# Optimization experiments

Measured on AMD Instinct MI355X. Metric: run time of the kernel, lower is better.

Reference implementation:

```python
import jax, jax.numpy as jnp
import numpy as np

N_BOXES = 1_000_000
EPS = 1e-6


def box2corners(box):
    """(..., 5) [x,y,w,h,angle] -> (..., 4, 2) corners (mmcv box2corners)."""
    x, y, w, h, a = (box[..., i] for i in range(5))
    dx = jnp.asarray([0.5, -0.5, -0.5, 0.5], box.dtype) * w[..., None]  # (...,4)
    dy = jnp.asarray([0.5, 0.5, -0.5, -0.5], box.dtype) * h[..., None]
    cos, sin = jnp.cos(a)[..., None], jnp.sin(a)[..., None]
    cx = dx * cos - dy * sin + x[..., None]
    cy = dx * sin + dy * cos + y[..., None]
    return jnp.stack([cx, cy], axis=-1)


def box_intersection(c1, c2):
    """All 4x4 edge-pair segment intersections. c1,c2: (N,4,2).
    Returns pts (N,4,4,2), mask (N,4,4)."""
    roll = jnp.array([1, 2, 3, 0])
    line1 = jnp.concatenate([c1, c1[:, roll, :]], axis=-1)  # (N,4,4): x1,y1,x2,y2
    line2 = jnp.concatenate([c2, c2[:, roll, :]], axis=-1)
    l1 = line1[:, :, None, :]  # (N,4,1,4)
    l2 = line2[:, None, :, :]  # (N,1,4,4)
    x1, y1, x2, y2 = l1[..., 0], l1[..., 1], l1[..., 2], l1[..., 3]
    x3, y3, x4, y4 = l2[..., 0], l2[..., 1], l2[..., 2], l2[..., 3]
    num = (y4 - y3) * (x2 - x1) - (x4 - x3) * (y2 - y1)
    den_t = (x4 - x3) * (y1 - y3) - (y4 - y3) * (x1 - x3)
    safe = jnp.where(num == 0.0, 1.0, num)
    t = jnp.where(num == 0.0, -1.0, den_t / safe)
    mask_t = (t > 0) & (t < 1)
    den_u = (x2 - x1) * (y1 - y3) - (y2 - y1) * (x1 - x3)
    u = jnp.where(num == 0.0, -1.0, -den_u / safe)
    mask_u = (u > 0) & (u < 1)
    mask = mask_t & mask_u
    t2 = den_t / (num + 1e-8)
    pts = jnp.stack([x1 + t2 * (x2 - x1), y1 + t2 * (y2 - y1)], axis=-1)
    pts = pts * mask[..., None].astype(pts.dtype)
    return pts, mask


def box1_in_box2(c1, c2):
    """Which corners of c1 lie inside box c2. (N,4,2)x(N,4,2)->(N,4) bool."""
    a = c2[:, 0:1, :]
    b = c2[:, 1:2, :]
    d = c2[:, 3:4, :]
    ab, ad, am = b - a, d - a, c1 - a
    pab = jnp.sum(ab * am, -1) / jnp.sum(ab * ab, -1)
    pad_ = jnp.sum(ad * am, -1) / jnp.sum(ad * ad, -1)
    e = 1e-6
    return (pab > -e) & (pab < 1 + e) & (pad_ > -e) & (pad_ < 1 + e)


def intersection_area(c1, c2):
    """Differentiable rotated-box intersection area via convex polygon clipping."""
    inter_pts, inter_mask = box_intersection(c1, c2)
    m1 = box1_in_box2(c1, c2)
    m2 = box1_in_box2(c2, c1)
    n = c1.shape[0]
    verts = jnp.concatenate([c1, c2, inter_pts.reshape(n, 16, 2)], axis=1)  # (N,24,2)
    mask = jnp.concatenate([m1, m2, inter_mask.reshape(n, 16)], axis=1)     # (N,24)
    k = jnp.sum(mask, axis=-1)  # num valid vertices per box
    mf = mask.astype(verts.dtype)
    mean = jnp.sum(verts * mf[..., None], axis=1, keepdims=True) / \
        jnp.maximum(k, 1).astype(verts.dtype)[:, None, None]
    vn = verts - mean
    # sort valid vertices counterclockwise by angle around centroid; invalid last
    ang = jnp.where(mask, jnp.arctan2(vn[..., 1], vn[..., 0]), 1e9)
    order = jnp.argsort(ang, axis=-1)
    vs = jnp.take_along_axis(verts, order[..., None], axis=1)  # (N,24,2)
    idx = jnp.arange(24)
    nxt = jnp.where(idx[None, :] + 1 < k[:, None], idx[None, :] + 1, 0)
    v_next = jnp.take_along_axis(vs, nxt[..., None], axis=1)
    cross = vs[..., 0] * v_next[..., 1] - vs[..., 1] * v_next[..., 0]
    valid = idx[None, :] < k[:, None]
    return jnp.abs(jnp.sum(jnp.where(valid, cross, 0.0), axis=-1)) * 0.5


def fpdiou_loss(pred, target):
    c1 = box2corners(pred)
    c2 = box2corners(target)
    inter = intersection_area(c1, c2)
    area1 = pred[:, 2] * pred[:, 3]
    area2 = target[:, 2] * target[:, 3]
    iou = inter / (area1 + area2 - inter)
    iou = jnp.maximum(iou, EPS)
    # corner-distance term (detached in original via .detach().cpu().numpy())
    p = jax.lax.stop_gradient(c1)
    g = jax.lax.stop_gradient(c2)
    ps = jnp.take_along_axis(p, jnp.argsort(p[..., 0], axis=-1)[..., None], axis=1)
    gs = jnp.take_along_axis(g, jnp.argsort(g[..., 0], axis=-1)[..., None], axis=1)
    d = 2.0 * (gs[:, 0, 0] - ps[:, 0, 0]) ** 2 \
        + (ps[:, 1, 0] - gs[:, 1, 0]) ** 2 + (ps[:, 1, 1] - gs[:, 1, 1]) ** 2 \
        + (ps[:, 2, 0] - gs[:, 2, 0]) ** 2 + (ps[:, 2, 1] - gs[:, 2, 1]) ** 2 \
        + (ps[:, 3, 0] - gs[:, 3, 0]) ** 2 + (ps[:, 3, 1] - gs[:, 3, 1]) ** 2
    res = d / (4.0 * 1024.0 ** 2)
    loss = 1.0 - iou + res  # mode='linear'
    return jnp.mean(loss)   # reduction='mean', loss_weight=1.0


def setup_inputs() -> dict:
    key = jax.random.key(0)
    k1, k2, k3, k4 = jax.random.split(key, 4)
    xy = jax.random.uniform(k1, (N_BOXES, 2), minval=0.0, maxval=1024.0)
    wh = jax.random.uniform(k2, (N_BOXES, 2), minval=8.0, maxval=96.0)
    ang = jax.random.uniform(k3, (N_BOXES, 1), minval=-np.pi / 2, maxval=np.pi / 2)
    pred = jnp.concatenate([xy, wh, ang], axis=-1).astype(jnp.float32)
    scale = jnp.asarray([4.0, 4.0, 3.0, 3.0, 0.1], jnp.float32)
    target = pred + jax.random.normal(k4, (N_BOXES, 5), jnp.float32) * scale
    target = target.at[:, 2:4].set(jnp.maximum(target[:, 2:4], 4.0))
    return {"pred": pred, "target": target}


def reference(pred, target):
    return fpdiou_loss(pred, target)
```

## Files before the change

kernel.cpp:

```cpp
#include <hip/hip_runtime.h>

#define BS 256
#define NS 24

__device__ __forceinline__ float rcpf(float x) { return __builtin_amdgcn_rcpf(x); }

__device__ __forceinline__ unsigned pk16(float x, float y) {
    unsigned r;
    asm("v_cvt_pknorm_i16_f32 %0, %1, %2" : "=v"(r) : "v"(x), "v"(y));
    return r;
}

#define CSWAPK(A, B) do {                                         \
    const unsigned ka_ = key[A], kb_ = key[B];                    \
    key[A] = ka_ < kb_ ? ka_ : kb_;                               \
    key[B] = ka_ < kb_ ? kb_ : ka_;                               \
} while (0)

#define CSW2(x, y, I, J) do {                                     \
    const bool sw_ = (x[J] < x[I]);                               \
    const float xi_ = x[I], xj_ = x[J], yi_ = y[I], yj_ = y[J];   \
    x[I] = sw_ ? xj_ : xi_;  x[J] = sw_ ? xi_ : xj_;              \
    y[I] = sw_ ? yj_ : yi_;  y[J] = sw_ ? yi_ : yj_;              \
} while (0)

__global__ __launch_bounds__(BS, 4)
void fpdiou_kernel(const float* __restrict__ pred, const float* __restrict__ tgt,
                   float* __restrict__ out, int n, float inv_n)
{
    __shared__ unsigned s_p[NS * BS];
    __shared__ float s_red[BS / 64];

    const int tid = threadIdx.x;
    const int i = blockIdx.x * BS + tid;
    float loss = 0.f;

    if (i < n) {
        const float* pp = pred + (size_t)i * 5;
        const float* gg = tgt  + (size_t)i * 5;
        const float p0 = pp[0], p1 = pp[1], pw = pp[2], ph = pp[3], pa = pp[4];
        const float g0 = gg[0], g1 = gg[1], gw = gg[2], gh = gg[3], ga = gg[4];

        const float s1 = __sinf(pa), co1 = __cosf(pa);
        const float s2 = __sinf(ga), co2 = __cosf(ga);

        const float DX[4] = {0.5f, -0.5f, -0.5f, 0.5f};
        const float DY[4] = {0.5f,  0.5f, -0.5f, -0.5f};
        float c1x[4], c1y[4], c2x[4], c2y[4];
#pragma unroll
        for (int q = 0; q < 4; q++) {
            float dx = DX[q] * pw, dy = DY[q] * ph;
            c1x[q] = dx * co1 - dy * s1 + p0;
            c1y[q] = dx * s1 + dy * co1 + p1;
            dx = DX[q] * gw; dy = DY[q] * gh;
            c2x[q] = dx * co2 - dy * s2 + g0;
            c2y[q] = dx * s2 + dy * co2 + g1;
        }

        const float PKS = 128.f / 32767.f;

        float res;
        {
            float px_[4] = {c1x[0], c1x[1], c1x[2], c1x[3]};
            float py_[4] = {c1y[0], c1y[1], c1y[2], c1y[3]};
            float gx_[4] = {c2x[0], c2x[1], c2x[2], c2x[3]};
            float gy_[4] = {c2y[0], c2y[1], c2y[2], c2y[3]};
            CSW2(px_, py_, 0, 1); CSW2(px_, py_, 2, 3);
            CSW2(px_, py_, 0, 2); CSW2(px_, py_, 1, 3); CSW2(px_, py_, 1, 2);
            CSW2(gx_, gy_, 0, 1); CSW2(gx_, gy_, 2, 3);
            CSW2(gx_, gy_, 0, 2); CSW2(gx_, gy_, 1, 3); CSW2(gx_, gy_, 1, 2);
            const float d0 = gx_[0] - px_[0];
            float d = 2.f * d0 * d0;
#pragma unroll
            for (int q = 1; q < 4; q++) {
                const float dxq = px_[q] - gx_[q];
                const float dyq = py_[q] - gy_[q];
                d += dxq * dxq + dyq * dyq;
            }
            res = d * (1.f / 4194304.f);
        }

        unsigned vm = 0;
        float sx = 0.f, sy = 0.f;
        const float e = 1e-6f;

        {
            const float ax = c2x[0], ay = c2y[0];
            const float abx = c2x[1] - ax, aby = c2y[1] - ay;
            const float adx = c2x[3] - ax, ady = c2y[3] - ay;
            const float dab = abx * abx + aby * aby;
            const float dad = adx * adx + ady * ady;
            const float lo_ab = -e * dab, hi_ab = (1.f + e) * dab;
            const float lo_ad = -e * dad, hi_ad = (1.f + e) * dad;
#pragma unroll
            for (int q = 0; q < 4; q++) {
                const float amx = c1x[q] - ax, amy = c1y[q] - ay;
                const float dot_ab = abx * amx + aby * amy;
                const float dot_ad = adx * amx + ady * amy;
                const bool m = (dot_ab > lo_ab) & (dot_ab < hi_ab)
                             & (dot_ad > lo_ad) & (dot_ad < hi_ad);
                s_p[q * BS + tid] = pk16((c1x[q] - p0) * PKS, (c1y[q] - p1) * PKS);
                if (m) { vm |= 1u << q; sx += c1x[q]; sy += c1y[q]; }
            }
        }
        {
            const float ax = c1x[0], ay = c1y[0];
            const float abx = c1x[1] - ax, aby = c1y[1] - ay;
            const float adx = c1x[3] - ax, ady = c1y[3] - ay;
            const float dab = abx * abx + aby * aby;
            const float dad = adx * adx + ady * ady;
            const float lo_ab = -e * dab, hi_ab = (1.f + e) * dab;
            const float lo_ad = -e * dad, hi_ad = (1.f + e) * dad;
#pragma unroll
            for (int q = 0; q < 4; q++) {
                const float amx = c2x[q] - ax, amy = c2y[q] - ay;
                const float dot_ab = abx * amx + aby * amy;
                const float dot_ad = adx * amx + ady * amy;
                const bool m = (dot_ab > lo_ab) & (dot_ab < hi_ab)
                             & (dot_ad > lo_ad) & (dot_ad < hi_ad);
                s_p[(4 + q) * BS + tid] = pk16((c2x[q] - p0) * PKS, (c2y[q] - p1) * PKS);
                if (m) { vm |= 1u << (4 + q); sx += c2x[q]; sy += c2y[q]; }
            }
        }
        float iix[16], iiy[16];
#pragma unroll
        for (int a = 0; a < 4; a++) {
            const float x1 = c1x[a], y1 = c1y[a];
            const float ex = c1x[(a + 1) & 3] - x1, ey = c1y[(a + 1) & 3] - y1;
#pragma unroll
            for (int b = 0; b < 4; b++) {
                const float x3 = c2x[b], y3 = c2y[b];
                const float fx = c2x[(b + 1) & 3] - x3, fy = c2y[(b + 1) & 3] - y3;
                const float num = fy * ex - fx * ey;
                const float dx13 = x1 - x3, dy13 = y1 - y3;
                const float den_t = fx * dy13 - fy * dx13;
                const float den_u = ex * dy13 - ey * dx13;
                const bool m = (den_t * num > 0.f) & (fabsf(den_t) < fabsf(num))
                             & (den_u * num < 0.f) & (fabsf(den_u) < fabsf(num));
                const float t2 = den_t * rcpf(num + 1e-8f);
                const float ix = fmaf(t2, ex, x1), iy = fmaf(t2, ey, y1);
                const int s = 8 + a * 4 + b;
                iix[a * 4 + b] = ix; iiy[a * 4 + b] = iy;
                s_p[s * BS + tid] = pk16((ix - p0) * PKS, (iy - p1) * PKS);
                if (m) { vm |= 1u << s; sx += ix; sy += iy; }
            }
        }

        const int kq = __popc(vm);
        const float kf = (float)(kq > 0 ? kq : 1);
        const float mx = sx * rcpf(kf), my = sy * rcpf(kf);
        unsigned key[NS];
#pragma unroll
        for (int s = 0; s < NS; s++) {
            const float vx = (s < 4) ? c1x[s] : (s < 8) ? c2x[s - 4] : iix[s - 8];
            const float vy = (s < 4) ? c1y[s] : (s < 8) ? c2y[s - 4] : iiy[s - 8];
            const float dx = vx - mx, dy = vy - my;
            const float sa = fabsf(dx) + fabsf(dy);
            const float m1 = fmaf(-dx, rcpf(sa), 1.f);
            float a4 = copysignf(m1, dy) + 4.f;
            a4 = ((vm >> s) & 1u) ? a4 : 1e9f;
            key[s] = (__float_as_uint(a4) & 0xFFFFFFE0u) | (unsigned)s;
        }

        CSWAPK(0,16); CSWAPK(1,17); CSWAPK(2,18); CSWAPK(3,19);
        CSWAPK(4,20); CSWAPK(5,21); CSWAPK(6,22); CSWAPK(7,23);
        CSWAPK(0,8);  CSWAPK(1,9);  CSWAPK(2,10); CSWAPK(3,11);
        CSWAPK(4,12); CSWAPK(5,13); CSWAPK(6,14); CSWAPK(7,15);
        CSWAPK(8,16); CSWAPK(9,17); CSWAPK(10,18); CSWAPK(11,19);
        CSWAPK(12,20); CSWAPK(13,21); CSWAPK(14,22); CSWAPK(15,23);
        CSWAPK(0,4);  CSWAPK(1,5);  CSWAPK(2,6);  CSWAPK(3,7);
        CSWAPK(8,12); CSWAPK(9,13); CSWAPK(10,14); CSWAPK(11,15);
        CSWAPK(16,20); CSWAPK(17,21); CSWAPK(18,22); CSWAPK(19,23);
        CSWAPK(4,16); CSWAPK(5,17); CSWAPK(6,18); CSWAPK(7,19);
        CSWAPK(4,8);  CSWAPK(5,9);  CSWAPK(6,10); CSWAPK(7,11);
        CSWAPK(12,16); CSWAPK(13,17); CSWAPK(14,18); CSWAPK(15,19);
        CSWAPK(0,2);  CSWAPK(1,3);  CSWAPK(4,6);  CSWAPK(5,7);
        CSWAPK(8,10); CSWAPK(9,11); CSWAPK(12,14); CSWAPK(13,15);
        CSWAPK(16,18); CSWAPK(17,19); CSWAPK(20,22); CSWAPK(21,23);
        CSWAPK(2,16); CSWAPK(3,17); CSWAPK(6,20); CSWAPK(7,21);
        CSWAPK(2,8);  CSWAPK(3,9);  CSWAPK(6,12); CSWAPK(7,13);
        CSWAPK(10,16); CSWAPK(11,17); CSWAPK(14,20); CSWAPK(15,21);
        CSWAPK(2,4);  CSWAPK(3,5);  CSWAPK(6,8);  CSWAPK(7,9);
        CSWAPK(10,12); CSWAPK(11,13); CSWAPK(14,16); CSWAPK(15,17);
        CSWAPK(18,20); CSWAPK(19,21);
        CSWAPK(0,1);  CSWAPK(2,3);  CSWAPK(4,5);  CSWAPK(6,7);
        CSWAPK(8,9);  CSWAPK(10,11); CSWAPK(12,13); CSWAPK(14,15);
        CSWAPK(16,17); CSWAPK(18,19); CSWAPK(20,21); CSWAPK(22,23);
        CSWAPK(1,16); CSWAPK(3,18); CSWAPK(5,20); CSWAPK(7,22);
        CSWAPK(1,8);  CSWAPK(3,10); CSWAPK(5,12); CSWAPK(7,14);
        CSWAPK(9,16); CSWAPK(11,18); CSWAPK(13,20); CSWAPK(15,22);
        CSWAPK(1,4);  CSWAPK(3,6);  CSWAPK(5,8);  CSWAPK(7,10);
        CSWAPK(9,12); CSWAPK(11,14); CSWAPK(13,16); CSWAPK(15,18);
        CSWAPK(17,20); CSWAPK(19,22);
        CSWAPK(1,2);  CSWAPK(3,4);  CSWAPK(5,6);  CSWAPK(7,8);
        CSWAPK(9,10); CSWAPK(11,12); CSWAPK(13,14); CSWAPK(15,16);
        CSWAPK(17,18); CSWAPK(19,20); CSWAPK(21,22);

        const unsigned s0 = key[0] & 31u;
        unsigned wv[NS];
#pragma unroll
        for (int j = 0; j < NS; j++) {
            const unsigned slot = (key[j] < 0x4E000000u) ? (key[j] & 31u) : s0;
            wv[j] = s_p[slot * BS + tid];
        }
        float X[NS + 1], Y[NS + 1];
#pragma unroll
        for (int j = 0; j < NS; j++) {
            X[j] = (float)((int)(wv[j] << 16) >> 16);
            Y[j] = (float)((int)wv[j] >> 16);
        }
        X[NS] = X[0]; Y[NS] = Y[0];
        float cr0 = 0.f, cr1 = 0.f, cr2 = 0.f;
#pragma unroll
        for (int j = 0; j < NS; j++) {
            const float t = X[j] * Y[j + 1] - Y[j] * X[j + 1];
            if ((j % 3) == 0) cr0 += t; else if ((j % 3) == 1) cr1 += t; else cr2 += t;
        }
        const float cr = (cr0 + cr1) + cr2;
        const float area = fabsf(cr) * (0.5f / 16384.f);

        const float a1 = pw * ph, a2 = gw * gh;
        const float iou = fmaxf(area * rcpf(a1 + a2 - area), 1e-6f);
        loss = 1.f - iou + res;
    }

#pragma unroll
    for (int off = 32; off > 0; off >>= 1)
        loss += __shfl_down(loss, off, 64);
    if ((tid & 63) == 0) s_red[tid >> 6] = loss;
    __syncthreads();
    if (tid == 0) {
        float t = 0.f;
#pragma unroll
        for (int w = 0; w < BS / 64; w++) t += s_red[w];
        atomicAdd(out, t * inv_n);
    }
}

extern "C" void kernel_launch(void* const* d_in, const int* in_sizes, int n_in,
                              void* d_out, int out_size, void* d_ws, size_t ws_size,
                              hipStream_t stream)
{
    const float* pred = (const float*)d_in[0];
    const float* tgt  = (const float*)d_in[1];
    float* out = (float*)d_out;
    const int n = in_sizes[0] / 5;
    const int nblk = (n + BS - 1) / BS;

    hipMemsetAsync(out, 0, sizeof(float), stream);
    fpdiou_kernel<<<nblk, BS, 0, stream>>>(pred, tgt, out, n, 1.f / (float)n);
}
```

Before: 134.8 us.

## Carry packed vertex payload through sorting network instead of LDS gather

Drops the shared-memory staging array for packed vertex coordinates and instead carries each packed 16-bit vertex as a register payload through the sorting network, swapping it alongside its key. Angle keys are now computed from the quantized packed coordinates relative to a quantized centroid rather than from full-precision vertices. This removes 24 LDS stores and 24 gathered loads per thread, and launch bounds are raised to target 8 blocks per CU. The cost is twice the select work in the sort, more register pressure under a tighter occupancy bound, and slightly lower precision in the angle keys.

```diff
diff --git a/kernel.cpp b/kernel.cpp
--- a/kernel.cpp
+++ b/kernel.cpp
@@ -11,10 +11,12 @@
     return r;
 }
 
-#define CSWAPK(A, B) do {                                         \
+#define CSWAPKP(A, B) do {                                        \
     const unsigned ka_ = key[A], kb_ = key[B];                    \
-    key[A] = ka_ < kb_ ? ka_ : kb_;                               \
-    key[B] = ka_ < kb_ ? kb_ : ka_;                               \
+    const unsigned pa_ = pay[A], pb_ = pay[B];                    \
+    const bool sw_ = (kb_ < ka_);                                 \
+    key[A] = sw_ ? kb_ : ka_;  key[B] = sw_ ? ka_ : kb_;          \
+    pay[A] = sw_ ? pb_ : pa_;  pay[B] = sw_ ? pa_ : pb_;          \
 } while (0)
 
 #define CSW2(x, y, I, J) do {                                     \
@@ -24,11 +26,10 @@
     y[I] = sw_ ? yj_ : yi_;  y[J] = sw_ ? yi_ : yj_;              \
 } while (0)
 
-__global__ __launch_bounds__(BS, 4)
+__global__ __launch_bounds__(BS, 8)
 void fpdiou_kernel(const float* __restrict__ pred, const float* __restrict__ tgt,
                    float* __restrict__ out, int n, float inv_n)
 {
-    __shared__ unsigned s_p[NS * BS];
     __shared__ float s_red[BS / 64];
 
     const int tid = threadIdx.x;
@@ -80,6 +81,7 @@
             res = d * (1.f / 4194304.f);
         }
 
+        unsigned pay[NS];
         unsigned vm = 0;
         float sx = 0.f, sy = 0.f;
         const float e = 1e-6f;
@@ -99,7 +101,7 @@
                 const float dot_ad = adx * amx + ady * amy;
                 const bool m = (dot_ab > lo_ab) & (dot_ab < hi_ab)
                              & (dot_ad > lo_ad) & (dot_ad < hi_ad);
-                s_p[q * BS + tid] = pk16((c1x[q] - p0) * PKS, (c1y[q] - p1) * PKS);
+                pay[q] = pk16((c1x[q] - p0) * PKS, (c1y[q] - p1) * PKS);
                 if (m) { vm |= 1u << q; sx += c1x[q]; sy += c1y[q]; }
             }
         }
@@ -118,11 +120,10 @@
                 const float dot_ad = adx * amx + ady * amy;
                 const bool m = (dot_ab > lo_ab) & (dot_ab < hi_ab)
                              & (dot_ad > lo_ad) & (dot_ad < hi_ad);
-                s_p[(4 + q) * BS + tid] = pk16((c2x[q] - p0) * PKS, (c2y[q] - p1) * PKS);
+                pay[4 + q] = pk16((c2x[q] - p0) * PKS, (c2y[q] - p1) * PKS);
                 if (m) { vm |= 1u << (4 + q); sx += c2x[q]; sy += c2y[q]; }
             }
         }
-        float iix[16], iiy[16];
 #pragma unroll
         for (int a = 0; a < 4; a++) {
             const float x1 = c1x[a], y1 = c1y[a];
@@ -140,21 +141,22 @@
                 const float t2 = den_t * rcpf(num + 1e-8f);
                 const float ix = fmaf(t2, ex, x1), iy = fmaf(t2, ey, y1);
                 const int s = 8 + a * 4 + b;
-                iix[a * 4 + b] = ix; iiy[a * 4 + b] = iy;
-                s_p[s * BS + tid] = pk16((ix - p0) * PKS, (iy - p1) * PKS);
+                pay[s] = pk16((ix - p0) * PKS, (iy - p1) * PKS);
                 if (m) { vm |= 1u << s; sx += ix; sy += iy; }
             }
         }
 
         const int kq = __popc(vm);
         const float kf = (float)(kq > 0 ? kq : 1);
-        const float mx = sx * rcpf(kf), my = sy * rcpf(kf);
+        const float rkf = rcpf(kf);
+        const float oxq = (sx * rkf - p0) * 128.f;
+        const float oyq = (sy * rkf - p1) * 128.f;
         unsigned key[NS];
 #pragma unroll
         for (int s = 0; s < NS; s++) {
-            const float vx = (s < 4) ? c1x[s] : (s < 8) ? c2x[s - 4] : iix[s - 8];
-            const float vy = (s < 4) ? c1y[s] : (s < 8) ? c2y[s - 4] : iiy[s - 8];
-            const float dx = vx - mx, dy = vy - my;
+            const unsigned w = pay[s];
+            const float dx = (float)((int)(w << 16) >> 16) - oxq;
+            const float dy = (float)((int)w >> 16) - oyq;
             const float sa = fabsf(dx) + fabsf(dy);
             const float m1 = fmaf(-dx, rcpf(sa), 1.f);
             float a4 = copysignf(m1, dy) + 4.f;
@@ -162,52 +164,47 @@
             key[s] = (__float_as_uint(a4) & 0xFFFFFFE0u) | (unsigned)s;
         }
 
-        CSWAPK(0,16); CSWAPK(1,17); CSWAPK(2,18); CSWAPK(3,19);
-        CSWAPK(4,20); CSWAPK(5,21); CSWAPK(6,22); CSWAPK(7,23);
-        CSWAPK(0,8);  CSWAPK(1,9);  CSWAPK(2,10); CSWAPK(3,11);
-        CSWAPK(4,12); CSWAPK(5,13); CSWAPK(6,14); CSWAPK(7,15);
-        CSWAPK(8,16); CSWAPK(9,17); CSWAPK(10,18); CSWAPK(11,19);
-        CSWAPK(12,20); CSWAPK(13,21); CSWAPK(14,22); CSWAPK(15,23);
-        CSWAPK(0,4);  CSWAPK(1,5);  CSWAPK(2,6);  CSWAPK(3,7);
-        CSWAPK(8,12); CSWAPK(9,13); CSWAPK(10,14); CSWAPK(11,15);
-        CSWAPK(16,20); CSWAPK(17,21); CSWAPK(18,22); CSWAPK(19,23);
-        CSWAPK(4,16); CSWAPK(5,17); CSWAPK(6,18); CSWAPK(7,19);
-        CSWAPK(4,8);  CSWAPK(5,9);  CSWAPK(6,10); CSWAPK(7,11);
-        CSWAPK(12,16); CSWAPK(13,17); CSWAPK(14,18); CSWAPK(15,19);
-        CSWAPK(0,2);  CSWAPK(1,3);  CSWAPK(4,6);  CSWAPK(5,7);
-        CSWAPK(8,10); CSWAPK(9,11); CSWAPK(12,14); CSWAPK(13,15);
-        CSWAPK(16,18); CSWAPK(17,19); CSWAPK(20,22); CSWAPK(21,23);
-        CSWAPK(2,16); CSWAPK(3,17); CSWAPK(6,20); CSWAPK(7,21);
-        CSWAPK(2,8);  CSWAPK(3,9);  CSWAPK(6,12); CSWAPK(7,13);
-        CSWAPK(10,16); CSWAPK(11,17); CSWAPK(14,20); CSWAPK(15,21);
-        CSWAPK(2,4);  CSWAPK(3,5);  CSWAPK(6,8);  CSWAPK(7,9);
-        CSWAPK(10,12); CSWAPK(11,13); CSWAPK(14,16); CSWAPK(15,17);
-        CSWAPK(18,20); CSWAPK(19,21);
-        CSWAPK(0,1);  CSWAPK(2,3);  CSWAPK(4,5);  CSWAPK(6,7);
-        CSWAPK(8,9);  CSWAPK(10,11); CSWAPK(12,13); CSWAPK(14,15);
-        CSWAPK(16,17); CSWAPK(18,19); CSWAPK(20,21); CSWAPK(22,23);
-        CSWAPK(1,16); CSWAPK(3,18); CSWAPK(5,20); CSWAPK(7,22);
-        CSWAPK(1,8);  CSWAPK(3,10); CSWAPK(5,12); CSWAPK(7,14);
-        CSWAPK(9,16); CSWAPK(11,18); CSWAPK(13,20); CSWAPK(15,22);
-        CSWAPK(1,4);  CSWAPK(3,6);  CSWAPK(5,8);  CSWAPK(7,10);
-        CSWAPK(9,12); CSWAPK(11,14); CSWAPK(13,16); CSWAPK(15,18);
-        CSWAPK(17,20); CSWAPK(19,22);
-        CSWAPK(1,2);  CSWAPK(3,4);  CSWAPK(5,6);  CSWAPK(7,8);
-        CSWAPK(9,10); CSWAPK(11,12); CSWAPK(13,14); CSWAPK(15,16);
-        CSWAPK(17,18); CSWAPK(19,20); CSWAPK(21,22);
-
-        const unsigned s0 = key[0] & 31u;
-        unsigned wv[NS];
+        CSWAPKP(0,16); CSWAPKP(1,17); CSWAPKP(2,18); CSWAPKP(3,19);
+        CSWAPKP(4,20); CSWAPKP(5,21); CSWAPKP(6,22); CSWAPKP(7,23);
+        CSWAPKP(0,8);  CSWAPKP(1,9);  CSWAPKP(2,10); CSWAPKP(3,11);
+        CSWAPKP(4,12); CSWAPKP(5,13); CSWAPKP(6,14); CSWAPKP(7,15);
+        CSWAPKP(8,16); CSWAPKP(9,17); CSWAPKP(10,18); CSWAPKP(11,19);
+        CSWAPKP(12,20); CSWAPKP(13,21); CSWAPKP(14,22); CSWAPKP(15,23);
+        CSWAPKP(0,4);  CSWAPKP(1,5);  CSWAPKP(2,6);  CSWAPKP(3,7);
+        CSWAPKP(8,12); CSWAPKP(9,13); CSWAPKP(10,14); CSWAPKP(11,15);
+        CSWAPKP(16,20); CSWAPKP(17,21); CSWAPKP(18,22); CSWAPKP(19,23);
+        CSWAPKP(4,16); CSWAPKP(5,17); CSWAPKP(6,18); CSWAPKP(7,19);
+        CSWAPKP(4,8);  CSWAPKP(5,9);  CSWAPKP(6,10); CSWAPKP(7,11);
+        CSWAPKP(12,16); CSWAPKP(13,17); CSWAPKP(14,18); CSWAPKP(15,19);
+        CSWAPKP(0,2);  CSWAPKP(1,3);  CSWAPKP(4,6);  CSWAPKP(5,7);
+        CSWAPKP(8,10); CSWAPKP(9,11); CSWAPKP(12,14); CSWAPKP(13,15);
+        CSWAPKP(16,18); CSWAPKP(17,19); CSWAPKP(20,22); CSWAPKP(21,23);
+        CSWAPKP(2,16); CSWAPKP(3,17); CSWAPKP(6,20); CSWAPKP(7,21);
+        CSWAPKP(2,8);  CSWAPKP(3,9);  CSWAPKP(6,12); CSWAPKP(7,13);
+        CSWAPKP(10,16); CSWAPKP(11,17); CSWAPKP(14,20); CSWAPKP(15,21);
+        CSWAPKP(2,4);  CSWAPKP(3,5);  CSWAPKP(6,8);  CSWAPKP(7,9);
+        CSWAPKP(10,12); CSWAPKP(11,13); CSWAPKP(14,16); CSWAPKP(15,17);
+        CSWAPKP(18,20); CSWAPKP(19,21);
+        CSWAPKP(0,1);  CSWAPKP(2,3);  CSWAPKP(4,5);  CSWAPKP(6,7);
+        CSWAPKP(8,9);  CSWAPKP(10,11); CSWAPKP(12,13); CSWAPKP(14,15);
+        CSWAPKP(16,17); CSWAPKP(18,19); CSWAPKP(20,21); CSWAPKP(22,23);
+        CSWAPKP(1,16); CSWAPKP(3,18); CSWAPKP(5,20); CSWAPKP(7,22);
+        CSWAPKP(1,8);  CSWAPKP(3,10); CSWAPKP(5,12); CSWAPKP(7,14);
+        CSWAPKP(9,16); CSWAPKP(11,18); CSWAPKP(13,20); CSWAPKP(15,22);
+        CSWAPKP(1,4);  CSWAPKP(3,6);  CSWAPKP(5,8);  CSWAPKP(7,10);
+        CSWAPKP(9,12); CSWAPKP(11,14); CSWAPKP(13,16); CSWAPKP(15,18);
+        CSWAPKP(17,20); CSWAPKP(19,22);
+        CSWAPKP(1,2);  CSWAPKP(3,4);  CSWAPKP(5,6);  CSWAPKP(7,8);
+        CSWAPKP(9,10); CSWAPKP(11,12); CSWAPKP(13,14); CSWAPKP(15,16);
+        CSWAPKP(17,18); CSWAPKP(19,20); CSWAPKP(21,22);
+
+        const unsigned pv0 = pay[0];
+        float X[NS + 1], Y[NS + 1];
 #pragma unroll
         for (int j = 0; j < NS; j++) {
-            const unsigned slot = (key[j] < 0x4E000000u) ? (key[j] & 31u) : s0;
-            wv[j] = s_p[slot * BS + tid];
-        }
-        float X[NS + 1], Y[NS + 1];
-#pragma unroll
-        for (int j = 0; j < NS; j++) {
-            X[j] = (float)((int)(wv[j] << 16) >> 16);
-            Y[j] = (float)((int)wv[j] >> 16);
+            const unsigned pv = (key[j] < 0x4E000000u) ? pay[j] : pv0;
+            X[j] = (float)((int)(pv << 16) >> 16);
+            Y[j] = (float)((int)pv >> 16);
         }
         X[NS] = X[0]; Y[NS] = Y[0];
         float cr0 = 0.f, cr1 = 0.f, cr2 = 0.f;
```

Measured after the change: 314.3 us. 2.33x slower.

## Pack quantized vertex coords into sort keys, eliminating LDS scratch

Applied to the files above, without the earlier changes.

Drops the shared-memory array of packed int16 vertex coordinates. Each vertex is now quantized to a 10-bit x and 10-bit y on a quarter-unit grid relative to the pred center, and these bits sit directly in the sort key, with a 12-bit quantized pseudo-angle in the top bits. After the sorting network the shoelace area is computed straight from the key bits, so the LDS stores, the gather loads and the separate float vertex arrays all go away. The cost is coarser precision: angle keys have about 12 bits, coordinates are 0.25-unit fixed point, and the 10-bit coordinate range wraps for large boxes or distant targets, which can distort the area.

```diff
diff --git a/kernel.cpp b/kernel.cpp
--- a/kernel.cpp
+++ b/kernel.cpp
@@ -4,12 +4,6 @@
 #define NS 24
 
 __device__ __forceinline__ float rcpf(float x) { return __builtin_amdgcn_rcpf(x); }
-
-__device__ __forceinline__ unsigned pk16(float x, float y) {
-    unsigned r;
-    asm("v_cvt_pknorm_i16_f32 %0, %1, %2" : "=v"(r) : "v"(x), "v"(y));
-    return r;
-}
 
 #define CSWAPK(A, B) do {                                         \
     const unsigned ka_ = key[A], kb_ = key[B];                    \
@@ -28,7 +22,6 @@
 void fpdiou_kernel(const float* __restrict__ pred, const float* __restrict__ tgt,
                    float* __restrict__ out, int n, float inv_n)
 {
-    __shared__ unsigned s_p[NS * BS];
     __shared__ float s_red[BS / 64];
 
     const int tid = threadIdx.x;
@@ -57,7 +50,8 @@
             c2y[q] = dx * s2 + dy * co2 + g1;
         }
 
-        const float PKS = 128.f / 32767.f;
+        const float bxc = 512.5f - 4.f * p0;
+        const float byc = 512.5f - 4.f * p1;
 
         float res;
         {
@@ -80,6 +74,7 @@
             res = d * (1.f / 4194304.f);
         }
 
+        unsigned key[NS];
         unsigned vm = 0;
         float sx = 0.f, sy = 0.f;
         const float e = 1e-6f;
@@ -99,7 +94,9 @@
                 const float dot_ad = adx * amx + ady * amy;
                 const bool m = (dot_ab > lo_ab) & (dot_ab < hi_ab)
                              & (dot_ad > lo_ad) & (dot_ad < hi_ad);
-                s_p[q * BS + tid] = pk16((c1x[q] - p0) * PKS, (c1y[q] - p1) * PKS);
+                const unsigned xb = (unsigned)(int)fmaf(c1x[q], 4.f, bxc) & 1023u;
+                const unsigned yb = (unsigned)(int)fmaf(c1y[q], 4.f, byc) & 1023u;
+                key[q] = (xb << 10) | yb;
                 if (m) { vm |= 1u << q; sx += c1x[q]; sy += c1y[q]; }
             }
         }
@@ -118,11 +115,12 @@
                 const float dot_ad = adx * amx + ady * amy;
                 const bool m = (dot_ab > lo_ab) & (dot_ab < hi_ab)
                              & (dot_ad > lo_ad) & (dot_ad < hi_ad);
-                s_p[(4 + q) * BS + tid] = pk16((c2x[q] - p0) * PKS, (c2y[q] - p1) * PKS);
+                const unsigned xb = (unsigned)(int)fmaf(c2x[q], 4.f, bxc) & 1023u;
+                const unsigned yb = (unsigned)(int)fmaf(c2y[q], 4.f, byc) & 1023u;
+                key[4 + q] = (xb << 10) | yb;
                 if (m) { vm |= 1u << (4 + q); sx += c2x[q]; sy += c2y[q]; }
             }
         }
-        float iix[16], iiy[16];
 #pragma unroll
         for (int a = 0; a < 4; a++) {
             const float x1 = c1x[a], y1 = c1y[a];
@@ -140,26 +138,29 @@
                 const float t2 = den_t * rcpf(num + 1e-8f);
                 const float ix = fmaf(t2, ex, x1), iy = fmaf(t2, ey, y1);
                 const int s = 8 + a * 4 + b;
-                iix[a * 4 + b] = ix; iiy[a * 4 + b] = iy;
-                s_p[s * BS + tid] = pk16((ix - p0) * PKS, (iy - p1) * PKS);
+                const unsigned xb = (unsigned)(int)fmaf(ix, 4.f, bxc) & 1023u;
+                const unsigned yb = (unsigned)(int)fmaf(iy, 4.f, byc) & 1023u;
+                key[s] = (xb << 10) | yb;
                 if (m) { vm |= 1u << s; sx += ix; sy += iy; }
             }
         }
 
         const int kq = __popc(vm);
         const float kf = (float)(kq > 0 ? kq : 1);
-        const float mx = sx * rcpf(kf), my = sy * rcpf(kf);
-        unsigned key[NS];
+        const float rkf = rcpf(kf);
+        const float mxq = fmaf(sx * rkf, 4.f, bxc - 0.5f);
+        const float myq = fmaf(sy * rkf, 4.f, byc - 0.5f);
 #pragma unroll
         for (int s = 0; s < NS; s++) {
-            const float vx = (s < 4) ? c1x[s] : (s < 8) ? c2x[s - 4] : iix[s - 8];
-            const float vy = (s < 4) ? c1y[s] : (s < 8) ? c2y[s - 4] : iiy[s - 8];
-            const float dx = vx - mx, dy = vy - my;
+            const unsigned w = key[s];
+            const float dx = (float)((w >> 10) & 1023u) - mxq;
+            const float dy = (float)(w & 1023u) - myq;
             const float sa = fabsf(dx) + fabsf(dy);
             const float m1 = fmaf(-dx, rcpf(sa), 1.f);
-            float a4 = copysignf(m1, dy) + 4.f;
-            a4 = ((vm >> s) & 1u) ? a4 : 1e9f;
-            key[s] = (__float_as_uint(a4) & 0xFFFFFFE0u) | (unsigned)s;
+            const float a4 = copysignf(m1, dy) + 2.f;
+            unsigned aq = (unsigned)(int)(a4 * 1023.f);
+            aq = ((vm >> s) & 1u) ? aq : 4095u;
+            key[s] = w | (aq << 20);
         }
 
         CSWAPK(0,16); CSWAPK(1,17); CSWAPK(2,18); CSWAPK(3,19);
@@ -196,28 +197,22 @@
         CSWAPK(9,10); CSWAPK(11,12); CSWAPK(13,14); CSWAPK(15,16);
         CSWAPK(17,18); CSWAPK(19,20); CSWAPK(21,22);
 
-        const unsigned s0 = key[0] & 31u;
-        unsigned wv[NS];
-#pragma unroll
-        for (int j = 0; j < NS; j++) {
-            const unsigned slot = (key[j] < 0x4E000000u) ? (key[j] & 31u) : s0;
-            wv[j] = s_p[slot * BS + tid];
-        }
-        float X[NS + 1], Y[NS + 1];
-#pragma unroll
-        for (int j = 0; j < NS; j++) {
-            X[j] = (float)((int)(wv[j] << 16) >> 16);
-            Y[j] = (float)((int)wv[j] >> 16);
-        }
-        X[NS] = X[0]; Y[NS] = Y[0];
+        const unsigned k0 = key[0];
+        const float fx0 = (float)((k0 >> 10) & 1023u);
+        const float fy0 = (float)(k0 & 1023u);
+        float xp = fx0, yp = fy0;
         float cr0 = 0.f, cr1 = 0.f, cr2 = 0.f;
 #pragma unroll
-        for (int j = 0; j < NS; j++) {
-            const float t = X[j] * Y[j + 1] - Y[j] * X[j + 1];
+        for (int j = 1; j < NS; j++) {
+            const unsigned w = (key[j] < 0xFFF00000u) ? key[j] : k0;
+            const float xc = (float)((w >> 10) & 1023u);
+            const float yc = (float)(w & 1023u);
+            const float t = xp * yc - yp * xc;
             if ((j % 3) == 0) cr0 += t; else if ((j % 3) == 1) cr1 += t; else cr2 += t;
-        }
-        const float cr = (cr0 + cr1) + cr2;
-        const float area = fabsf(cr) * (0.5f / 16384.f);
+            xp = xc; yp = yc;
+        }
+        const float cr = (cr0 + cr1) + (cr2 + (xp * fy0 - yp * fx0));
+        const float area = fabsf(cr) * 0.03125f;
 
         const float a1 = pw * ph, a2 = gw * gh;
         const float iou = fmaxf(area * rcpf(a1 + a2 - area), 1e-6f);
```

After: 132.9 us. No clear change (-1.4%).
